# Performance work log

Hardware: AMD Instinct MI355X
Metric: run time of the kernel (lower is better)

Reference implementation:

```python
import jax, jax.numpy as jnp
import numpy as np

N = 100000   # nodes
E = 1600000  # edges
D = 128      # input feature dim
H = 128      # hidden dim
C = 40       # output classes


def _gcn_conv(x, W, b, src, dst, norm):
    # PyG GCNConv: h = x @ W; out_i = sum_j (d_i^-1/2 d_j^-1/2) h_j over in-edges,
    # including self-loops, then + bias. norm = deg^-1/2 with self-loop-augmented degree.
    h = x @ W                                    # [N, H]
    coef = norm[src] * norm[dst]                 # [E]
    agg = jax.ops.segment_sum(h[src] * coef[:, None], dst, num_segments=N)
    agg = agg + h * (norm * norm)[:, None]       # self-loop term
    return agg + b


def setup_inputs() -> dict:
    key = jax.random.key(0)
    ks = jax.random.split(key, 12)
    x = jax.random.normal(ks[0], (N, D), dtype=jnp.float32)
    edge_index = jax.random.randint(ks[1], (2, E), 0, N, dtype=jnp.int64)

    def lin(k, fan_in, fan_out):
        s = 1.0 / np.sqrt(fan_in)
        return jax.random.uniform(k, (fan_in, fan_out), jnp.float32, -s, s)

    return {
        "x": x,
        "edge_index": edge_index,
        "W1": lin(ks[2], D, H), "b1": jnp.zeros((H,), jnp.float32),
        "W2": lin(ks[3], H, H), "b2": jnp.zeros((H,), jnp.float32),
        "W3": lin(ks[4], H, H), "b3": jnp.zeros((H,), jnp.float32),
        "Wp1": lin(ks[5], H, H), "bp1": jnp.zeros((H,), jnp.float32),
        "Wp2": lin(ks[6], H, C), "bp2": jnp.zeros((C,), jnp.float32),
    }


def reference(x, edge_index, W1, b1, W2, b2, W3, b3, Wp1, bp1, Wp2, bp2):
    src, dst = edge_index[0], edge_index[1]
    # degree with self-loops (GCNConv adds self-loops by default)
    deg = jax.ops.segment_sum(jnp.ones((E,), jnp.float32), dst, num_segments=N) + 1.0
    norm = jax.lax.rsqrt(deg)                    # deg^-1/2

    h = x
    for W, b in ((W1, b1), (W2, b2), (W3, b3)):
        h = _gcn_conv(h, W, b, src, dst, norm)
        h = jax.nn.relu(h)
        # dropout is a no-op at inference / rate 0

    h = h @ Wp1 + bp1
    h = h @ Wp2 + bp2
    return jax.nn.log_softmax(h, axis=1)
```

## Files before the change

### kernel.cpp

```cpp
#include <hip/hip_runtime.h>
#include <hip/hip_bf16.h>
#include <math.h>


#define DH 128
#define NC 40
#define BN 256
#define MAXNB 512
#define CH 8192
#define ECAP 6144
#define SP 136

typedef __attribute__((ext_vector_type(8))) short bf16x8;
typedef __attribute__((ext_vector_type(4))) float f32x4;

__device__ __forceinline__ unsigned short f2bf(float f) {
    unsigned u = __float_as_uint(f);
    unsigned r = (u + 0x7fffu + ((u >> 16) & 1u)) >> 16;
    return (unsigned short)r;
}
__device__ __forceinline__ unsigned pack2(float lo, float hi) {
    return (unsigned)f2bf(lo) | ((unsigned)f2bf(hi) << 16);
}


__global__ __launch_bounds__(256) void bucket_hist(const int* __restrict__ dst, int E,
                                                   unsigned* __restrict__ bcnt) {
    __shared__ unsigned h[MAXNB];
    int tid = threadIdx.x;
    for (int i = tid; i < MAXNB; i += 256) h[i] = 0;
    __syncthreads();
    int e0 = blockIdx.x * CH;
    int e1 = min(e0 + CH, E);
    for (int i = e0 + tid; i < e1; i += 256)
        atomicAdd(&h[dst[i] >> 8], 1u);
    __syncthreads();
    for (int i = tid; i < MAXNB; i += 256)
        if (h[i]) atomicAdd(&bcnt[i], h[i]);
}

__global__ __launch_bounds__(256) void bucket_alloc(const unsigned* __restrict__ bcnt,
                                                    unsigned* __restrict__ bbase,
                                                    unsigned* __restrict__ bpos,
                                                    unsigned* __restrict__ cursor, int NB) {
    int i = blockIdx.x * 256 + threadIdx.x;
    if (i < NB) {
        unsigned c = bcnt[i];
        unsigned o = atomicAdd(cursor, c);
        bbase[i] = o;
        bpos[i] = o;
    }
}

__global__ __launch_bounds__(256) void bucket_scatter(const int* __restrict__ src,
                                                      const int* __restrict__ dst, int E,
                                                      unsigned* __restrict__ bpos,
                                                      unsigned* __restrict__ ebuf) {
    __shared__ unsigned hist[MAXNB];
    __shared__ unsigned lbase[MAXNB];
    __shared__ unsigned gbase[MAXNB];
    __shared__ unsigned cur[MAXNB];
    __shared__ unsigned sorted[CH];
    __shared__ unsigned short sbkt[CH];
    __shared__ unsigned total;

    int tid = threadIdx.x;
    int e0 = blockIdx.x * CH;
    int nE = min(CH, E - e0);

    for (int i = tid; i < MAXNB; i += 256) { hist[i] = 0; cur[i] = 0; }
    if (tid == 0) total = 0;
    __syncthreads();

    for (int i = tid; i < nE; i += 256)
        atomicAdd(&hist[dst[e0 + i] >> 8], 1u);
    __syncthreads();

    for (int i = tid; i < MAXNB; i += 256) {
        unsigned h = hist[i];
        lbase[i] = h ? atomicAdd(&total, h) : 0u;
        gbase[i] = h ? atomicAdd(&bpos[i], h) : 0u;
    }
    __syncthreads();

    for (int i = tid; i < nE; i += 256) {
        int s = src[e0 + i];
        int d = dst[e0 + i];
        unsigned b = (unsigned)d >> 8;
        unsigned r = atomicAdd(&cur[b], 1u);
        unsigned p = lbase[b] + r;
        sorted[p] = ((unsigned)s << 8) | ((unsigned)d & 255u);
        sbkt[p] = (unsigned short)b;
    }
    __syncthreads();

    for (int p = tid; p < nE; p += 256) {
        unsigned b = sbkt[p];
        ebuf[gbase[b] + (p - lbase[b])] = sorted[p];
    }
}

__global__ __launch_bounds__(256) void bucket_csr(const unsigned* __restrict__ ebuf,
                                                  const unsigned* __restrict__ bbase,
                                                  const unsigned* __restrict__ bcnt,
                                                  unsigned* __restrict__ off,
                                                  unsigned* __restrict__ cnt,
                                                  float* __restrict__ nrm,
                                                  int* __restrict__ csr, int N) {
    __shared__ unsigned h[BN];
    __shared__ unsigned nb[BN];
    __shared__ unsigned ncur[BN];
    __shared__ int lcsr[ECAP];
    __shared__ unsigned tot;

    int b = blockIdx.x;
    int tid = threadIdx.x;
    unsigned ebase = bbase[b];
    unsigned ecnt = bcnt[b];

    h[tid] = 0;
    if (tid == 0) tot = 0;
    __syncthreads();

    for (unsigned i = tid; i < ecnt; i += 256)
        atomicAdd(&h[ebuf[ebase + i] & 255u], 1u);
    __syncthreads();

    unsigned myh = h[tid];
    unsigned mybase = myh ? atomicAdd(&tot, myh) : 0u;
    nb[tid] = mybase;
    ncur[tid] = 0;
    int node = b * BN + tid;
    if (node < N) {
        off[node] = ebase + mybase;
        cnt[node] = myh;
        nrm[node] = rsqrtf((float)myh + 1.0f);
    }
    __syncthreads();

    if (ecnt <= ECAP) {
        for (unsigned i = tid; i < ecnt; i += 256) {
            unsigned v = ebuf[ebase + i];
            unsigned nl = v & 255u;
            unsigned r = atomicAdd(&ncur[nl], 1u);
            lcsr[nb[nl] + r] = (int)(v >> 8);
        }
        __syncthreads();
        for (unsigned i = tid; i < ecnt; i += 256)
            csr[ebase + i] = lcsr[i];
    } else {
        for (unsigned i = tid; i < ecnt; i += 256) {
            unsigned v = ebuf[ebase + i];
            unsigned nl = v & 255u;
            unsigned r = atomicAdd(&ncur[nl], 1u);
            csr[ebase + nb[nl] + r] = (int)(v >> 8);
        }
    }
}


__global__ __launch_bounds__(256) void deg_hist(const unsigned* __restrict__ cnt, int N,
                                                unsigned* __restrict__ dh) {
    __shared__ unsigned h[256];
    int t = threadIdx.x;
    h[t] = 0;
    __syncthreads();
    int i = blockIdx.x * 256 + t;
    if (i < N) atomicAdd(&h[min(cnt[i], 255u)], 1u);
    __syncthreads();
    if (h[t]) atomicAdd(&dh[t], h[t]);
}

__global__ __launch_bounds__(256) void deg_scan(const unsigned* __restrict__ dh,
                                                unsigned* __restrict__ binpos) {
    __shared__ unsigned s[256];
    int t = threadIdx.x;
    s[t] = dh[t];
    __syncthreads();
    unsigned sum = 0;
    for (int d = t + 1; d < 256; ++d) sum += s[d];
    binpos[t] = sum;
}

__global__ __launch_bounds__(256) void deg_scatter(const unsigned* __restrict__ cnt, int N,
                                                   unsigned* __restrict__ binpos,
                                                   int* __restrict__ perm) {
    __shared__ unsigned h[256], base[256], cur[256];
    int t = threadIdx.x;
    h[t] = 0; cur[t] = 0;
    __syncthreads();
    int i = blockIdx.x * 256 + t;
    unsigned d = 0;
    if (i < N) { d = min(cnt[i], 255u); atomicAdd(&h[d], 1u); }
    __syncthreads();
    if (h[t]) base[t] = atomicAdd(&binpos[t], h[t]);
    __syncthreads();
    if (i < N) {
        unsigned r = atomicAdd(&cur[d], 1u);
        perm[base[d] + r] = i;
    }
}


__global__ __launch_bounds__(256) void prep_w(const float* __restrict__ W1,
                                              const float* __restrict__ W2,
                                              const float* __restrict__ W3,
                                              const float* __restrict__ Wp1,
                                              const float* __restrict__ bp1,
                                              const float* __restrict__ Wp2,
                                              const float* __restrict__ bp2,
                                              unsigned short* __restrict__ Wt,
                                              unsigned short* __restrict__ Wft,
                                              float* __restrict__ bfh) {
    int id = blockIdx.x * 256 + threadIdx.x;
    if (id < 3 * DH * DH) {
        int l = id >> 14, r = id & (DH * DH - 1);
        int k = r >> 7, n = r & 127;
        const float* W = (l == 0) ? W1 : (l == 1) ? W2 : W3;
        Wt[l * DH * DH + n * DH + k] = f2bf(W[k * DH + n]);
    } else if (id < 3 * DH * DH + 48 * DH) {
        int o = id - 3 * DH * DH;
        int c = o >> 7, k = o & 127;
        float acc = 0.f;
        if (c < NC)
            for (int j = 0; j < DH; ++j) acc += Wp1[k * DH + j] * Wp2[j * NC + c];
        Wft[c * DH + k] = f2bf(acc);
    } else if (id < 3 * DH * DH + 48 * DH + 48) {
        int c = id - 3 * DH * DH - 48 * DH;
        float acc = 0.f;
        if (c < NC) {
            acc = bp2[c];
            for (int j = 0; j < DH; ++j) acc += bp1[j] * Wp2[j * NC + c];
        }
        bfh[c] = acc;
    }
}


__global__ __launch_bounds__(256) void gemm_mfma_f32(const float* __restrict__ X,
                                                     const unsigned short* __restrict__ Wt,
                                                     const float* __restrict__ nrm,
                                                     unsigned short* __restrict__ outb,
                                                     int nrows) {
    const int tid = threadIdx.x;
    const int wave = tid >> 6;
    const int lane = tid & 63;
    const int m = lane & 15;
    const int quad = lane >> 4;
    const int rbase = blockIdx.x * 128 + wave * 32;

    union U8 { bf16x8 v; unsigned u[4]; };

    f32x4 acc[2][8];
#pragma unroll
    for (int rt = 0; rt < 2; ++rt)
#pragma unroll
        for (int ct = 0; ct < 8; ++ct) acc[rt][ct] = (f32x4){0.f, 0.f, 0.f, 0.f};

#pragma unroll
    for (int kt = 0; kt < 4; ++kt) {
        const int kof = kt * 32 + quad * 8;
        bf16x8 a[2], b[8];
#pragma unroll
        for (int rt = 0; rt < 2; ++rt) {
            int r = rbase + rt * 16 + m;
            r = (r < nrows) ? r : (nrows - 1);
            const float* p = X + (size_t)r * DH + kof;
            float4 u0 = *(const float4*)p;
            float4 u1 = *(const float4*)(p + 4);
            U8 t;
            t.u[0] = pack2(u0.x, u0.y);
            t.u[1] = pack2(u0.z, u0.w);
            t.u[2] = pack2(u1.x, u1.y);
            t.u[3] = pack2(u1.z, u1.w);
            a[rt] = t.v;
        }
#pragma unroll
        for (int ct = 0; ct < 8; ++ct)
            b[ct] = *(const bf16x8*)(Wt + (ct * 16 + m) * DH + kof);
#pragma unroll
        for (int rt = 0; rt < 2; ++rt)
#pragma unroll
            for (int ct = 0; ct < 8; ++ct)
                acc[rt][ct] = __builtin_amdgcn_mfma_f32_16x16x32_bf16(a[rt], b[ct], acc[rt][ct], 0, 0, 0);
    }

#pragma unroll
    for (int rt = 0; rt < 2; ++rt)
#pragma unroll
        for (int reg = 0; reg < 4; ++reg) {
            int r = rbase + rt * 16 + quad * 4 + reg;
            if (r < nrows) {
                float s = nrm[r];
#pragma unroll
                for (int ct = 0; ct < 8; ++ct)
                    outb[(size_t)r * DH + ct * 16 + m] = f2bf(acc[rt][ct][reg] * s);
            }
        }
}


__device__ __forceinline__ void bf8_add(float* acc, uint4 v) {
    acc[0] += __uint_as_float(v.x << 16);
    acc[1] += __uint_as_float(v.x & 0xffff0000u);
    acc[2] += __uint_as_float(v.y << 16);
    acc[3] += __uint_as_float(v.y & 0xffff0000u);
    acc[4] += __uint_as_float(v.z << 16);
    acc[5] += __uint_as_float(v.z & 0xffff0000u);
    acc[6] += __uint_as_float(v.w << 16);
    acc[7] += __uint_as_float(v.w & 0xffff0000u);
}

__device__ __forceinline__ void gather_phase(const uint4* __restrict__ Abf,
                                             const int* __restrict__ csr,
                                             const unsigned* __restrict__ off,
                                             const unsigned* __restrict__ cnt,
                                             const float* __restrict__ nrm,
                                             const float* __restrict__ bias,
                                             const int* __restrict__ perm,
                                             unsigned short (*sA)[SP], int N) {
    const int tid = threadIdx.x;
    const int g = tid >> 4;
    const int lane = tid & 15;
    const int idx = blockIdx.x * 16 + g;
    if (idx < N) {
        const int node = perm[idx];
        float acc[8];
        {
            uint4 v = Abf[(size_t)node * 16 + lane];
            acc[0] = __uint_as_float(v.x << 16);
            acc[1] = __uint_as_float(v.x & 0xffff0000u);
            acc[2] = __uint_as_float(v.y << 16);
            acc[3] = __uint_as_float(v.y & 0xffff0000u);
            acc[4] = __uint_as_float(v.z << 16);
            acc[5] = __uint_as_float(v.z & 0xffff0000u);
            acc[6] = __uint_as_float(v.w << 16);
            acc[7] = __uint_as_float(v.w & 0xffff0000u);
        }
        unsigned o = off[node];
        unsigned d = cnt[node];

        unsigned e = 0;
        for (; e + 4 <= d; e += 4) {
            int s0 = csr[o + e + 0];
            int s1 = csr[o + e + 1];
            int s2 = csr[o + e + 2];
            int s3 = csr[o + e + 3];
            uint4 v0 = Abf[(size_t)s0 * 16 + lane];
            uint4 v1 = Abf[(size_t)s1 * 16 + lane];
            uint4 v2 = Abf[(size_t)s2 * 16 + lane];
            uint4 v3 = Abf[(size_t)s3 * 16 + lane];
            bf8_add(acc, v0);
            bf8_add(acc, v1);
            bf8_add(acc, v2);
            bf8_add(acc, v3);
        }
        for (; e < d; ++e) {
            int s = csr[o + e];
            uint4 v = Abf[(size_t)s * 16 + lane];
            bf8_add(acc, v);
        }

        float nm = nrm[node];
        float4 b0 = *(const float4*)(bias + lane * 8);
        float4 b1 = *(const float4*)(bias + lane * 8 + 4);
        unsigned short* p = &sA[g][lane * 8];
        p[0] = f2bf(fmaxf(acc[0] * nm + b0.x, 0.f));
        p[1] = f2bf(fmaxf(acc[1] * nm + b0.y, 0.f));
        p[2] = f2bf(fmaxf(acc[2] * nm + b0.z, 0.f));
        p[3] = f2bf(fmaxf(acc[3] * nm + b0.w, 0.f));
        p[4] = f2bf(fmaxf(acc[4] * nm + b1.x, 0.f));
        p[5] = f2bf(fmaxf(acc[5] * nm + b1.y, 0.f));
        p[6] = f2bf(fmaxf(acc[6] * nm + b1.z, 0.f));
        p[7] = f2bf(fmaxf(acc[7] * nm + b1.w, 0.f));
    }
    __syncthreads();
}


__global__ __launch_bounds__(256) void agg_gemm(const uint4* __restrict__ Abf,
                                                const int* __restrict__ csr,
                                                const unsigned* __restrict__ off,
                                                const unsigned* __restrict__ cnt,
                                                const float* __restrict__ nrm,
                                                const float* __restrict__ bias,
                                                const int* __restrict__ perm,
                                                const unsigned short* __restrict__ Wt,
                                                unsigned short* __restrict__ outb, int N) {
    __shared__ unsigned short sA[16][SP];
    gather_phase(Abf, csr, off, cnt, nrm, bias, perm, sA, N);

    const int tid = threadIdx.x;
    const int wave = tid >> 6;
    const int l64 = tid & 63;
    const int m = l64 & 15;
    const int quad = l64 >> 4;

    f32x4 acc[2];
    acc[0] = (f32x4){0.f, 0.f, 0.f, 0.f};
    acc[1] = (f32x4){0.f, 0.f, 0.f, 0.f};

#pragma unroll
    for (int kt = 0; kt < 4; ++kt) {
        const int kof = kt * 32 + quad * 8;
        bf16x8 a = *(const bf16x8*)&sA[m][kof];
#pragma unroll
        for (int c2 = 0; c2 < 2; ++c2) {
            const int ct = wave * 2 + c2;
            bf16x8 b = *(const bf16x8*)(Wt + (ct * 16 + m) * DH + kof);
            acc[c2] = __builtin_amdgcn_mfma_f32_16x16x32_bf16(a, b, acc[c2], 0, 0, 0);
        }
    }

#pragma unroll
    for (int reg = 0; reg < 4; ++reg) {
        int idx = blockIdx.x * 16 + quad * 4 + reg;
        if (idx < N) {
            int r = perm[idx];
            float s = nrm[r];
#pragma unroll
            for (int c2 = 0; c2 < 2; ++c2)
                outb[(size_t)r * DH + (wave * 2 + c2) * 16 + m] = f2bf(acc[c2][reg] * s);
        }
    }
}


__global__ __launch_bounds__(256) void agg_head(const uint4* __restrict__ Abf,
                                                const int* __restrict__ csr,
                                                const unsigned* __restrict__ off,
                                                const unsigned* __restrict__ cnt,
                                                const float* __restrict__ nrm,
                                                const float* __restrict__ bias,
                                                const int* __restrict__ perm,
                                                const unsigned short* __restrict__ Wft,
                                                const float* __restrict__ bfh,
                                                float* __restrict__ out, int N) {
    __shared__ unsigned short sA[16][SP];
    gather_phase(Abf, csr, off, cnt, nrm, bias, perm, sA, N);

    const int tid = threadIdx.x;
    if (tid >= 64) return;
    const int m = tid & 15;
    const int quad = tid >> 4;

    f32x4 acc[3];
#pragma unroll
    for (int ct = 0; ct < 3; ++ct) acc[ct] = (f32x4){0.f, 0.f, 0.f, 0.f};

#pragma unroll
    for (int kt = 0; kt < 4; ++kt) {
        const int kof = kt * 32 + quad * 8;
        bf16x8 a = *(const bf16x8*)&sA[m][kof];
#pragma unroll
        for (int ct = 0; ct < 3; ++ct) {
            bf16x8 b = *(const bf16x8*)(Wft + (ct * 16 + m) * DH + kof);
            acc[ct] = __builtin_amdgcn_mfma_f32_16x16x32_bf16(a, b, acc[ct], 0, 0, 0);
        }
    }

    float bias0 = bfh[m];
    float bias1 = bfh[16 + m];
    float bias2 = bfh[32 + m];

#pragma unroll
    for (int reg = 0; reg < 4; ++reg) {
        float v0 = acc[0][reg] + bias0;
        float v1 = acc[1][reg] + bias1;
        float v2 = (m < 8) ? (acc[2][reg] + bias2) : -1e30f;
        float mx = fmaxf(fmaxf(v0, v1), v2);
#pragma unroll
        for (int dlt = 1; dlt < 16; dlt <<= 1) mx = fmaxf(mx, __shfl_xor(mx, dlt));
        float s = __expf(v0 - mx) + __expf(v1 - mx) + ((m < 8) ? __expf(v2 - mx) : 0.f);
#pragma unroll
        for (int dlt = 1; dlt < 16; dlt <<= 1) s += __shfl_xor(s, dlt);
        float ls = mx + __logf(s);
        int idx = blockIdx.x * 16 + quad * 4 + reg;
        if (idx < N) {
            int r = perm[idx];
            out[(size_t)r * NC + m] = v0 - ls;
            out[(size_t)r * NC + 16 + m] = v1 - ls;
            if (m < 8) out[(size_t)r * NC + 32 + m] = v2 - ls;
        }
    }
}


extern "C" void kernel_launch(void* const* d_in, const int* in_sizes, int n_in,
                              void* d_out, int out_size, void* d_ws, size_t ws_size,
                              hipStream_t stream) {
    const float* x   = (const float*)d_in[0];
    const int*   ei  = (const int*)d_in[1];
    const float* W1  = (const float*)d_in[2];
    const float* b1  = (const float*)d_in[3];
    const float* W2  = (const float*)d_in[4];
    const float* b2  = (const float*)d_in[5];
    const float* W3  = (const float*)d_in[6];
    const float* b3  = (const float*)d_in[7];
    const float* Wp1 = (const float*)d_in[8];
    const float* bp1 = (const float*)d_in[9];
    const float* Wp2 = (const float*)d_in[10];
    const float* bp2 = (const float*)d_in[11];
    float* out = (float*)d_out;

    const int N = in_sizes[0] / DH;
    const int E = in_sizes[1] / 2;
    const int* src = ei;
    const int* dst = ei + E;
    const int NB = (N + BN - 1) / BN;

    char* w = (char*)d_ws;
    unsigned short* Ab  = (unsigned short*)w; w += (size_t)N * DH * 2;
    unsigned short* Bb  = (unsigned short*)w; w += (size_t)N * DH * 2;
    int*      csr    = (int*)w;      w += (size_t)E * 4;
    unsigned* ebuf   = (unsigned*)w; w += (size_t)E * 4;
    unsigned* bcnt   = (unsigned*)w; w += MAXNB * 4;
    unsigned* cursor = (unsigned*)w; w += 16;
    unsigned* dh     = (unsigned*)w; w += 256 * 4;
    unsigned* bbase  = (unsigned*)w; w += MAXNB * 4;
    unsigned* bpos   = (unsigned*)w; w += MAXNB * 4;
    unsigned* binpos = (unsigned*)w; w += 256 * 4;
    unsigned* off    = (unsigned*)w; w += (size_t)N * 4;
    unsigned* cnt    = (unsigned*)w; w += (size_t)N * 4;
    float*    nrm    = (float*)w;    w += (size_t)N * 4;
    int*      perm   = (int*)w;      w += (size_t)((N + 31) & ~31) * 4;
    unsigned short* Wt  = (unsigned short*)w; w += 3 * DH * DH * 2;
    unsigned short* Wft = (unsigned short*)w; w += 48 * DH * 2;
    float*    bfh    = (float*)w;    w += 64 * 4;

    const int gC = (E + CH - 1) / CH;
    const int gN = (N + 255) / 256;

    hipMemsetAsync(bcnt, 0, MAXNB * 4 + 16 + 256 * 4, stream);
    bucket_hist   <<<gC, 256, 0, stream>>>(dst, E, bcnt);
    bucket_alloc  <<<(NB + 255) / 256, 256, 0, stream>>>(bcnt, bbase, bpos, cursor, NB);
    bucket_scatter<<<gC, 256, 0, stream>>>(src, dst, E, bpos, ebuf);
    bucket_csr    <<<NB, 256, 0, stream>>>(ebuf, bbase, bcnt, off, cnt, nrm, csr, N);
    deg_hist      <<<gN, 256, 0, stream>>>(cnt, N, dh);
    deg_scan      <<<1, 256, 0, stream>>>(dh, binpos);
    deg_scatter   <<<gN, 256, 0, stream>>>(cnt, N, binpos, perm);
    prep_w<<<(3 * DH * DH + 48 * DH + 48 + 255) / 256, 256, 0, stream>>>(
        W1, W2, W3, Wp1, bp1, Wp2, bp2, Wt, Wft, bfh);

    const int gG = (N + 127) / 128;
    const int gF = (N + 15) / 16;

    gemm_mfma_f32<<<gG, 256, 0, stream>>>(x, Wt, nrm, Ab, N);
    agg_gemm<<<gF, 256, 0, stream>>>((const uint4*)Ab, csr, off, cnt, nrm, b1, perm,
                                     Wt + DH * DH, Bb, N);
    agg_gemm<<<gF, 256, 0, stream>>>((const uint4*)Bb, csr, off, cnt, nrm, b2, perm,
                                     Wt + 2 * DH * DH, Ab, N);
    agg_head<<<gF, 256, 0, stream>>>((const uint4*)Ab, csr, off, cnt, nrm, b3, perm,
                                     Wft, bfh, out, N);
}
```

Before: 432.6 us.

## Lay out CSR in degree-sorted order and pack offset/degree per sorted index

The CSR is rebuilt so that neighbor lists are stored contiguously in degree-sorted (perm) order, and a packed offset/degree word per sorted index replaces the separate off/cnt/nrm lookups by node id in the aggregation kernels. Norm is recomputed from degree, node id and norm are cached in shared memory for the epilogue, and the bf16 store to shared memory is vectorised. The intent is fewer random dependent loads and better locality of csr reads in the three gather kernels, at the cost of an extra bucket pass and the assumption that offset fits in 23 bits.

Result: faster. 415.6 us (-3.9%).

```diff
diff --git a/kernel.cpp b/kernel.cpp
--- a/kernel.cpp
+++ b/kernel.cpp
@@ -100,104 +100,123 @@
     }
 }
 
-__global__ __launch_bounds__(256) void bucket_csr(const unsigned* __restrict__ ebuf,
+
+__global__ __launch_bounds__(256) void bucket_deg(const unsigned* __restrict__ ebuf,
                                                   const unsigned* __restrict__ bbase,
                                                   const unsigned* __restrict__ bcnt,
-                                                  unsigned* __restrict__ off,
                                                   unsigned* __restrict__ cnt,
                                                   float* __restrict__ nrm,
-                                                  int* __restrict__ csr, int N) {
+                                                  unsigned* __restrict__ dh, int N) {
     __shared__ unsigned h[BN];
-    __shared__ unsigned nb[BN];
-    __shared__ unsigned ncur[BN];
-    __shared__ int lcsr[ECAP];
-    __shared__ unsigned tot;
-
-    int b = blockIdx.x;
-    int tid = threadIdx.x;
-    unsigned ebase = bbase[b];
-    unsigned ecnt = bcnt[b];
-
-    h[tid] = 0;
-    if (tid == 0) tot = 0;
-    __syncthreads();
-
+    __shared__ unsigned dhh[256];
+    int b = blockIdx.x, tid = threadIdx.x;
+    unsigned ebase = bbase[b], ecnt = bcnt[b];
+    h[tid] = 0; dhh[tid] = 0;
+    __syncthreads();
     for (unsigned i = tid; i < ecnt; i += 256)
         atomicAdd(&h[ebuf[ebase + i] & 255u], 1u);
     __syncthreads();
-
+    int node = b * BN + tid;
     unsigned myh = h[tid];
-    unsigned mybase = myh ? atomicAdd(&tot, myh) : 0u;
-    nb[tid] = mybase;
-    ncur[tid] = 0;
-    int node = b * BN + tid;
     if (node < N) {
-        off[node] = ebase + mybase;
         cnt[node] = myh;
         nrm[node] = rsqrtf((float)myh + 1.0f);
-    }
+        atomicAdd(&dhh[min(myh, 255u)], 1u);
+    }
+    __syncthreads();
+    if (dhh[tid]) atomicAdd(&dh[tid], dhh[tid]);
+}
+
+__global__ __launch_bounds__(256) void deg_scan(const unsigned* __restrict__ dh,
+                                                unsigned* __restrict__ binpos,
+                                                unsigned* __restrict__ nstart0,
+                                                unsigned* __restrict__ estart) {
+    __shared__ unsigned s[256];
+    int t = threadIdx.x;
+    s[t] = dh[t];
+    __syncthreads();
+    unsigned ns = 0, es = 0;
+    for (int d = t + 1; d < 256; ++d) { ns += s[d]; es += s[d] * (unsigned)d; }
+    binpos[t] = ns;
+    nstart0[t] = ns;
+    estart[t] = es;
+}
+
+__global__ __launch_bounds__(256) void deg_scatter(const unsigned* __restrict__ cnt, int N,
+                                                   unsigned* __restrict__ binpos,
+                                                   const unsigned* __restrict__ nstart0,
+                                                   const unsigned* __restrict__ estart,
+                                                   int* __restrict__ perm,
+                                                   unsigned* __restrict__ pd2,
+                                                   unsigned* __restrict__ offN) {
+    __shared__ unsigned h[256], base[256], cur[256], sns[256], ses[256];
+    int t = threadIdx.x;
+    h[t] = 0; cur[t] = 0; sns[t] = nstart0[t]; ses[t] = estart[t];
+    __syncthreads();
+    int i = blockIdx.x * 256 + t;
+    unsigned d = 0;
+    if (i < N) { d = min(cnt[i], 255u); atomicAdd(&h[d], 1u); }
+    __syncthreads();
+    if (h[t]) base[t] = atomicAdd(&binpos[t], h[t]);
+    __syncthreads();
+    if (i < N) {
+        unsigned r = atomicAdd(&cur[d], 1u);
+        unsigned idx = base[d] + r;
+        unsigned off2 = ses[d] + (idx - sns[d]) * d;
+        perm[idx] = i;
+        pd2[idx] = (off2 << 9) | d;
+        offN[i] = off2;
+    }
+}
+
+
+__global__ __launch_bounds__(256) void bucket_fill(const unsigned* __restrict__ ebuf,
+                                                   const unsigned* __restrict__ bbase,
+                                                   const unsigned* __restrict__ bcnt,
+                                                   const unsigned* __restrict__ offN,
+                                                   int* __restrict__ csr, int N) {
+    __shared__ unsigned h[BN], lb[BN], cur[BN], ofs[BN];
+    __shared__ int lcsr[ECAP];
+    __shared__ unsigned char snl[ECAP];
+    __shared__ unsigned tot;
+
+    int b = blockIdx.x, tid = threadIdx.x;
+    unsigned ebase = bbase[b], ecnt = bcnt[b];
+    int node = b * BN + tid;
+    h[tid] = 0; cur[tid] = 0;
+    ofs[tid] = (node < N) ? offN[node] : 0u;
+    if (tid == 0) tot = 0;
+    __syncthreads();
+
+    for (unsigned i = tid; i < ecnt; i += 256)
+        atomicAdd(&h[ebuf[ebase + i] & 255u], 1u);
+    __syncthreads();
+
+    unsigned myh = h[tid];
+    lb[tid] = myh ? atomicAdd(&tot, myh) : 0u;
     __syncthreads();
 
     if (ecnt <= ECAP) {
         for (unsigned i = tid; i < ecnt; i += 256) {
             unsigned v = ebuf[ebase + i];
             unsigned nl = v & 255u;
-            unsigned r = atomicAdd(&ncur[nl], 1u);
-            lcsr[nb[nl] + r] = (int)(v >> 8);
+            unsigned r = atomicAdd(&cur[nl], 1u);
+            unsigned p = lb[nl] + r;
+            lcsr[p] = (int)(v >> 8);
+            snl[p] = (unsigned char)nl;
         }
         __syncthreads();
-        for (unsigned i = tid; i < ecnt; i += 256)
-            csr[ebase + i] = lcsr[i];
+        for (unsigned i = tid; i < ecnt; i += 256) {
+            unsigned nl = snl[i];
+            csr[ofs[nl] + (i - lb[nl])] = lcsr[i];
+        }
     } else {
         for (unsigned i = tid; i < ecnt; i += 256) {
             unsigned v = ebuf[ebase + i];
             unsigned nl = v & 255u;
-            unsigned r = atomicAdd(&ncur[nl], 1u);
-            csr[ebase + nb[nl] + r] = (int)(v >> 8);
-        }
-    }
-}
-
-
-__global__ __launch_bounds__(256) void deg_hist(const unsigned* __restrict__ cnt, int N,
-                                                unsigned* __restrict__ dh) {
-    __shared__ unsigned h[256];
-    int t = threadIdx.x;
-    h[t] = 0;
-    __syncthreads();
-    int i = blockIdx.x * 256 + t;
-    if (i < N) atomicAdd(&h[min(cnt[i], 255u)], 1u);
-    __syncthreads();
-    if (h[t]) atomicAdd(&dh[t], h[t]);
-}
-
-__global__ __launch_bounds__(256) void deg_scan(const unsigned* __restrict__ dh,
-                                                unsigned* __restrict__ binpos) {
-    __shared__ unsigned s[256];
-    int t = threadIdx.x;
-    s[t] = dh[t];
-    __syncthreads();
-    unsigned sum = 0;
-    for (int d = t + 1; d < 256; ++d) sum += s[d];
-    binpos[t] = sum;
-}
-
-__global__ __launch_bounds__(256) void deg_scatter(const unsigned* __restrict__ cnt, int N,
-                                                   unsigned* __restrict__ binpos,
-                                                   int* __restrict__ perm) {
-    __shared__ unsigned h[256], base[256], cur[256];
-    int t = threadIdx.x;
-    h[t] = 0; cur[t] = 0;
-    __syncthreads();
-    int i = blockIdx.x * 256 + t;
-    unsigned d = 0;
-    if (i < N) { d = min(cnt[i], 255u); atomicAdd(&h[d], 1u); }
-    __syncthreads();
-    if (h[t]) base[t] = atomicAdd(&binpos[t], h[t]);
-    __syncthreads();
-    if (i < N) {
-        unsigned r = atomicAdd(&cur[d], 1u);
-        perm[base[d] + r] = i;
+            unsigned r = atomicAdd(&cur[nl], 1u);
+            csr[ofs[nl] + r] = (int)(v >> 8);
+        }
     }
 }
 
@@ -313,18 +332,21 @@
 
 __device__ __forceinline__ void gather_phase(const uint4* __restrict__ Abf,
                                              const int* __restrict__ csr,
-                                             const unsigned* __restrict__ off,
-                                             const unsigned* __restrict__ cnt,
-                                             const float* __restrict__ nrm,
+                                             const unsigned* __restrict__ pd2,
+                                             const int* __restrict__ perm,
                                              const float* __restrict__ bias,
-                                             const int* __restrict__ perm,
-                                             unsigned short (*sA)[SP], int N) {
+                                             unsigned short (*sA)[SP],
+                                             int* snode, float* snrm, int N) {
     const int tid = threadIdx.x;
     const int g = tid >> 4;
     const int lane = tid & 15;
     const int idx = blockIdx.x * 16 + g;
     if (idx < N) {
+        const unsigned pd = pd2[idx];
+        const unsigned o = pd >> 9;
+        const unsigned d = pd & 511u;
         const int node = perm[idx];
+
         float acc[8];
         {
             uint4 v = Abf[(size_t)node * 16 + lane];
@@ -337,8 +359,6 @@
             acc[6] = __uint_as_float(v.w << 16);
             acc[7] = __uint_as_float(v.w & 0xffff0000u);
         }
-        unsigned o = off[node];
-        unsigned d = cnt[node];
 
         unsigned e = 0;
         for (; e + 4 <= d; e += 4) {
@@ -361,18 +381,16 @@
             bf8_add(acc, v);
         }
 
-        float nm = nrm[node];
+        float nm = rsqrtf((float)d + 1.0f);
+        if (lane == 0) { snode[g] = node; snrm[g] = nm; }
         float4 b0 = *(const float4*)(bias + lane * 8);
         float4 b1 = *(const float4*)(bias + lane * 8 + 4);
-        unsigned short* p = &sA[g][lane * 8];
-        p[0] = f2bf(fmaxf(acc[0] * nm + b0.x, 0.f));
-        p[1] = f2bf(fmaxf(acc[1] * nm + b0.y, 0.f));
-        p[2] = f2bf(fmaxf(acc[2] * nm + b0.z, 0.f));
-        p[3] = f2bf(fmaxf(acc[3] * nm + b0.w, 0.f));
-        p[4] = f2bf(fmaxf(acc[4] * nm + b1.x, 0.f));
-        p[5] = f2bf(fmaxf(acc[5] * nm + b1.y, 0.f));
-        p[6] = f2bf(fmaxf(acc[6] * nm + b1.z, 0.f));
-        p[7] = f2bf(fmaxf(acc[7] * nm + b1.w, 0.f));
+        uint4 ov;
+        ov.x = pack2(fmaxf(acc[0] * nm + b0.x, 0.f), fmaxf(acc[1] * nm + b0.y, 0.f));
+        ov.y = pack2(fmaxf(acc[2] * nm + b0.z, 0.f), fmaxf(acc[3] * nm + b0.w, 0.f));
+        ov.z = pack2(fmaxf(acc[4] * nm + b1.x, 0.f), fmaxf(acc[5] * nm + b1.y, 0.f));
+        ov.w = pack2(fmaxf(acc[6] * nm + b1.z, 0.f), fmaxf(acc[7] * nm + b1.w, 0.f));
+        *(uint4*)&sA[g][lane * 8] = ov;
     }
     __syncthreads();
 }
@@ -380,15 +398,15 @@
 
 __global__ __launch_bounds__(256) void agg_gemm(const uint4* __restrict__ Abf,
                                                 const int* __restrict__ csr,
-                                                const unsigned* __restrict__ off,
-                                                const unsigned* __restrict__ cnt,
-                                                const float* __restrict__ nrm,
+                                                const unsigned* __restrict__ pd2,
+                                                const int* __restrict__ perm,
                                                 const float* __restrict__ bias,
-                                                const int* __restrict__ perm,
                                                 const unsigned short* __restrict__ Wt,
                                                 unsigned short* __restrict__ outb, int N) {
     __shared__ unsigned short sA[16][SP];
-    gather_phase(Abf, csr, off, cnt, nrm, bias, perm, sA, N);
+    __shared__ int snode[16];
+    __shared__ float snrm[16];
+    gather_phase(Abf, csr, pd2, perm, bias, sA, snode, snrm, N);
 
     const int tid = threadIdx.x;
     const int wave = tid >> 6;
@@ -416,8 +434,8 @@
     for (int reg = 0; reg < 4; ++reg) {
         int idx = blockIdx.x * 16 + quad * 4 + reg;
         if (idx < N) {
-            int r = perm[idx];
-            float s = nrm[r];
+            int r = snode[quad * 4 + reg];
+            float s = snrm[quad * 4 + reg];
 #pragma unroll
             for (int c2 = 0; c2 < 2; ++c2)
                 outb[(size_t)r * DH + (wave * 2 + c2) * 16 + m] = f2bf(acc[c2][reg] * s);
@@ -428,16 +446,16 @@
 
 __global__ __launch_bounds__(256) void agg_head(const uint4* __restrict__ Abf,
                                                 const int* __restrict__ csr,
-                                                const unsigned* __restrict__ off,
-                                                const unsigned* __restrict__ cnt,
-                                                const float* __restrict__ nrm,
+                                                const unsigned* __restrict__ pd2,
+                                                const int* __restrict__ perm,
                                                 const float* __restrict__ bias,
-                                                const int* __restrict__ perm,
                                                 const unsigned short* __restrict__ Wft,
                                                 const float* __restrict__ bfh,
                                                 float* __restrict__ out, int N) {
     __shared__ unsigned short sA[16][SP];
-    gather_phase(Abf, csr, off, cnt, nrm, bias, perm, sA, N);
+    __shared__ int snode[16];
+    __shared__ float snrm[16];
+    gather_phase(Abf, csr, pd2, perm, bias, sA, snode, snrm, N);
 
     const int tid = threadIdx.x;
     if (tid >= 64) return;
@@ -477,7 +495,7 @@
         float ls = mx + __logf(s);
         int idx = blockIdx.x * 16 + quad * 4 + reg;
         if (idx < N) {
-            int r = perm[idx];
+            int r = snode[quad * 4 + reg];
             out[(size_t)r * NC + m] = v0 - ls;
             out[(size_t)r * NC + 16 + m] = v1 - ls;
             if (m < 8) out[(size_t)r * NC + 32 + m] = v2 - ls;
@@ -520,9 +538,12 @@
     unsigned* bbase  = (unsigned*)w; w += MAXNB * 4;
     unsigned* bpos   = (unsigned*)w; w += MAXNB * 4;
     unsigned* binpos = (unsigned*)w; w += 256 * 4;
-    unsigned* off    = (unsigned*)w; w += (size_t)N * 4;
+    unsigned* nstart0= (unsigned*)w; w += 256 * 4;
+    unsigned* estart = (unsigned*)w; w += 256 * 4;
     unsigned* cnt    = (unsigned*)w; w += (size_t)N * 4;
     float*    nrm    = (float*)w;    w += (size_t)N * 4;
+    unsigned* offN   = (unsigned*)w; w += (size_t)N * 4;
+    unsigned* pd2    = (unsigned*)w; w += (size_t)((N + 31) & ~31) * 4;
     int*      perm   = (int*)w;      w += (size_t)((N + 31) & ~31) * 4;
     unsigned short* Wt  = (unsigned short*)w; w += 3 * DH * DH * 2;
     unsigned short* Wft = (unsigned short*)w; w += 48 * DH * 2;
@@ -535,10 +556,10 @@
     bucket_hist   <<<gC, 256, 0, stream>>>(dst, E, bcnt);
     bucket_alloc  <<<(NB + 255) / 256, 256, 0, stream>>>(bcnt, bbase, bpos, cursor, NB);
     bucket_scatter<<<gC, 256, 0, stream>>>(src, dst, E, bpos, ebuf);
-    bucket_csr    <<<NB, 256, 0, stream>>>(ebuf, bbase, bcnt, off, cnt, nrm, csr, N);
-    deg_hist      <<<gN, 256, 0, stream>>>(cnt, N, dh);
-    deg_scan      <<<1, 256, 0, stream>>>(dh, binpos);
-    deg_scatter   <<<gN, 256, 0, stream>>>(cnt, N, binpos, perm);
+    bucket_deg    <<<NB, 256, 0, stream>>>(ebuf, bbase, bcnt, cnt, nrm, dh, N);
+    deg_scan      <<<1, 256, 0, stream>>>(dh, binpos, nstart0, estart);
+    deg_scatter   <<<gN, 256, 0, stream>>>(cnt, N, binpos, nstart0, estart, perm, pd2, offN);
+    bucket_fill   <<<NB, 256, 0, stream>>>(ebuf, bbase, bcnt, offN, csr, N);
     prep_w<<<(3 * DH * DH + 48 * DH + 48 + 255) / 256, 256, 0, stream>>>(
         W1, W2, W3, Wp1, bp1, Wp2, bp2, Wt, Wft, bfh);
 
@@ -546,10 +567,10 @@
     const int gF = (N + 15) / 16;
 
     gemm_mfma_f32<<<gG, 256, 0, stream>>>(x, Wt, nrm, Ab, N);
-    agg_gemm<<<gF, 256, 0, stream>>>((const uint4*)Ab, csr, off, cnt, nrm, b1, perm,
+    agg_gemm<<<gF, 256, 0, stream>>>((const uint4*)Ab, csr, pd2, perm, b1,
                                      Wt + DH * DH, Bb, N);
-    agg_gemm<<<gF, 256, 0, stream>>>((const uint4*)Bb, csr, off, cnt, nrm, b2, perm,
+    agg_gemm<<<gF, 256, 0, stream>>>((const uint4*)Bb, csr, pd2, perm, b2,
                                      Wt + 2 * DH * DH, Ab, N);
-    agg_head<<<gF, 256, 0, stream>>>((const uint4*)Ab, csr, off, cnt, nrm, b3, perm,
+    agg_head<<<gF, 256, 0, stream>>>((const uint4*)Ab, csr, pd2, perm, b3,
                                      Wft, bfh, out, N);
 }
```
